# Kernel optimization log

Hardware: AMD Instinct MI355X
Metric: run time of the kernel (lower is better)

## Reference

```python
import jax, jax.numpy as jnp
import numpy as np

B, N, FEAT, H, HID = 2, 2048, 128, 5, 3
D = H * HID  # 15
NEG_INF = -9e15


def _gat(x, adj, W, a, concat):
    # x: [B,N,Fin], W: [Fin,Fout], a: [2*Fout]
    Wh = jnp.einsum('bnf,fo->bno', x, W)
    Fo = W.shape[1]
    f1 = Wh @ a[:Fo]          # [B,N]
    f2 = Wh @ a[Fo:]          # [B,N]
    e = jax.nn.leaky_relu(f1[:, :, None] + f2[:, None, :], 0.2)  # [B,N,N]
    att = jax.nn.softmax(jnp.where(adj > 0, e, NEG_INF), axis=-1)
    h = jnp.einsum('bij,bjo->bio', att, Wh)
    return (jax.nn.elu(h) if concat else h), att


def _diff_pool(x, adj, s):
    # torch_geometric.dense_diff_pool
    s = jax.nn.softmax(s, axis=-1)                       # [B,N,K]
    out = jnp.einsum('bnk,bnf->bkf', s, x)               # [B,K,F]
    out_adj = jnp.einsum('bnk,bnm,bml->bkl', s, adj, s)  # [B,K,K]
    link = jnp.linalg.norm(adj - jnp.einsum('bnk,bmk->bnm', s, s)) / adj.size
    ent = jnp.mean(jnp.sum(-s * jnp.log(s + 1e-15), axis=-1))
    return out, out_adj, link, ent


def setup_inputs() -> dict:
    key = jax.random.key(0)
    ks = jax.random.split(key, 16)
    p = lambda k, shp: (jax.random.normal(k, shp, jnp.float32) * 0.1)
    d = {}
    d['x'] = jax.random.normal(ks[0], (B, N, FEAT), jnp.float32)
    d['adj'] = jax.random.bernoulli(ks[1], 0.05, (B, N, N)).astype(jnp.float32)
    d['W_heads'] = p(ks[2], (H, FEAT, HID))
    d['a_heads'] = p(ks[3], (H, 2 * HID))
    d['W_out'] = p(ks[4], (D, D)); d['a_out'] = p(ks[5], (2 * D,))
    d['W_p1'] = p(ks[6], (D, 32)); d['a_p1'] = p(ks[7], (64,))
    d['lin1_w'] = p(ks[8], (32, 32)); d['lin1_b'] = p(ks[9], (32,))
    d['W_p2'] = p(ks[10], (D, 4)); d['a_p2'] = p(ks[11], (8,))
    d['lin2_w'] = p(ks[12], (4, 4)); d['lin2_b'] = p(ks[13], (4,))
    d['lin_w'] = p(ks[14], (4 * D, 2)); d['lin_b'] = p(ks[15], (2,))
    return d


def reference(x, adj, W_heads, a_heads, W_out, a_out, W_p1, a_p1,
              lin1_w, lin1_b, W_p2, a_p2, lin2_w, lin2_b, lin_w, lin_b):
    # eval mode: dropout = identity
    hs, atts = jax.vmap(lambda W, a: _gat(x, adj, W, a, True))(W_heads, a_heads)
    # hs: [H,B,N,HID] -> concat heads -> [B,N,H*HID]
    h = jnp.moveaxis(hs, 0, 2).reshape(x.shape[0], x.shape[1], -1)
    h = jax.nn.elu(_gat(h, adj, W_out, a_out, False)[0])
    # pool 1: N -> 32 clusters
    s1 = _gat(h, adj, W_p1, a_p1, True)[0] @ lin1_w + lin1_b
    h, adj2, link1, ent1 = _diff_pool(h, adj, s1)
    # pool 2: 32 -> 4 clusters
    s2 = _gat(h, adj2, W_p2, a_p2, True)[0] @ lin2_w + lin2_b
    h, adj3, link2, ent2 = _diff_pool(h, adj2, s2)
    ypred = h.reshape(h.shape[0], -1) @ lin_w + lin_b  # [B, class_num]
    loss = link1 + link2
    return ypred, loss, atts
```

## Files before the change

### kernel.cpp

```cpp
#include <hip/hip_runtime.h>
#include <hip/hip_bf16.h>

#define NN 2048
#define BB 2
#define RB 4096
#define CAP 192

__device__ __forceinline__ float lrelu(float v) { return v > 0.f ? v : 0.2f * v; }
__device__ __forceinline__ float eluf(float v) { return v > 0.f ? v : __expf(v) - 1.f; }

__device__ __forceinline__ float wredsum(float v) {
    for (int o = 32; o; o >>= 1) v += __shfl_down(v, o, 64);
    return v;
}
__device__ __forceinline__ float wredmax(float v) {
    for (int o = 32; o; o >>= 1) v = fmaxf(v, __shfl_down(v, o, 64));
    return v;
}
__device__ __forceinline__ float bsum(float v) {
    for (int m = 32; m; m >>= 1) v += __shfl_xor(v, m, 64);
    return v;
}
__device__ __forceinline__ float bmax(float v) {
    for (int m = 32; m; m >>= 1) v = fmaxf(v, __shfl_xor(v, m, 64));
    return v;
}

__global__ void k_zero(float* S) { if (threadIdx.x < 2) S[threadIdx.x] = 0.f; }

__global__ __launch_bounds__(128) void k_prep1(const float* __restrict__ x,
                                               const float* __restrict__ W,
                                               const float* __restrict__ a,
                                               float* __restrict__ Wh1,
                                               float* __restrict__ f1o,
                                               float* __restrict__ f2o) {
    __shared__ float xl[128];
    __shared__ float whl[15];
    const int r = blockIdx.x, t = threadIdx.x;
    xl[t] = x[(size_t)r * 128 + t];
    __syncthreads();
    if (t < 15) {
        const int h = t / 3, f = t % 3;
        float acc = 0.f;
        const float* Wp = W + (size_t)h * 128 * 3 + f;
        for (int k = 0; k < 128; k++) acc += xl[k] * Wp[k * 3];
        whl[t] = acc;
        Wh1[((size_t)h * RB + r) * 3 + f] = acc;
    }
    __syncthreads();
    if (t < 10) {
        const int h = t >> 1, which = t & 1;
        const float* ah = a + h * 6 + which * 3;
        float acc = whl[h * 3] * ah[0] + whl[h * 3 + 1] * ah[1] + whl[h * 3 + 2] * ah[2];
        (which ? f2o : f1o)[h * RB + r] = acc;
    }
}

__global__ __launch_bounds__(256) void k_gat1(const float* __restrict__ adj,
                                              const float* __restrict__ Wh,
                                              const float* __restrict__ f1,
                                              const float* __restrict__ f2,
                                              const float* __restrict__ W_out,
                                              const float* __restrict__ a_out,
                                              float* __restrict__ Wh2,
                                              float* __restrict__ f1_2,
                                              float* __restrict__ f2_2,
                                              float* __restrict__ att_out,
                                              int* __restrict__ nnzcnt,
                                              unsigned short* __restrict__ nnzidx,
                                              float* __restrict__ S) {
    __shared__ float al[NN];
    __shared__ float red[64];
    __shared__ float h1row[15];
    __shared__ unsigned short nidx[CAP];
    __shared__ int ncnt;
    const int tid = threadIdx.x, wid = tid >> 6, lane = tid & 63;
    const int r = blockIdx.x;
    const int b = r >> 11, i = r & (NN - 1);
    const float* arow = adj + ((size_t)b * NN + i) * NN;

    if (tid == 0) ncnt = 0;
    __syncthreads();

    float a2p = 0.f;
    for (int j = tid; j < NN; j += 256) {
        const float a = arow[j];
        al[j] = a;
        a2p += a * a;
        if (a > 0.f) {
            const int pos = atomicAdd(&ncnt, 1);
            if (pos < CAP) nidx[pos] = (unsigned short)j;
        }
    }
    a2p = wredsum(a2p);
    if (lane == 0) red[wid] = a2p;
    __syncthreads();
    if (tid == 0) atomicAdd(S, red[0] + red[1] + red[2] + red[3]);
    const int cnt = min(ncnt, CAP);
    if (tid == 0) nnzcnt[r] = cnt;
    for (int p = tid; p < cnt; p += 256) nnzidx[(size_t)r * CAP + p] = nidx[p];
    __syncthreads();

    for (int h = 0; h < 5; ++h) {
        const float f1i = f1[h * RB + r];
        const float* f2h = f2 + h * RB + b * NN;
        const float* WhB = Wh + ((size_t)h * RB + b * NN) * 3;

        float ereg[8];
        float lmax = -3.0e38f;
#pragma unroll
        for (int it = 0; it < 8; ++it) {
            const int j = tid + it * 256;
            const float e = (al[j] > 0.f) ? lrelu(f1i + f2h[j]) : -9.0e15f;
            ereg[it] = e;
            lmax = fmaxf(lmax, e);
        }
        lmax = wredmax(lmax);
        if (lane == 0) red[wid] = lmax;
        __syncthreads();
        const float m = fmaxf(fmaxf(red[0], red[1]), fmaxf(red[2], red[3]));
        __syncthreads();

        float lsum = 0.f, h0 = 0.f, h1v = 0.f, h2v = 0.f;
#pragma unroll
        for (int it = 0; it < 8; ++it) {
            const int j = tid + it * 256;
            const float p = __expf(ereg[it] - m);
            ereg[it] = p;
            lsum += p;
            if (p > 0.f) {
                const float* w = WhB + (size_t)j * 3;
                h0 += p * w[0]; h1v += p * w[1]; h2v += p * w[2];
            }
        }
        lsum = wredsum(lsum);
        if (lane == 0) red[wid] = lsum;
        __syncthreads();
        const float inv = 1.f / (red[0] + red[1] + red[2] + red[3]);

        float* ao = att_out + (((size_t)h * BB + b) * NN + i) * NN;
#pragma unroll
        for (int it = 0; it < 8; ++it) ao[tid + it * 256] = ereg[it] * inv;
        __syncthreads();

        h0 = wredsum(h0); h1v = wredsum(h1v); h2v = wredsum(h2v);
        if (lane == 0) { red[wid * 3] = h0; red[wid * 3 + 1] = h1v; red[wid * 3 + 2] = h2v; }
        __syncthreads();
        if (tid < 3) {
            const float v = (red[tid] + red[3 + tid] + red[6 + tid] + red[9 + tid]) * inv;
            h1row[h * 3 + tid] = eluf(v);
        }
        __syncthreads();
    }

    if (wid == 0) {
        float whv = 0.f;
        if (lane < 15) {
#pragma unroll
            for (int f = 0; f < 15; f++) whv += h1row[f] * W_out[f * 15 + lane];
            Wh2[(size_t)r * 15 + lane] = whv;
        }
        float s1p = (lane < 15) ? whv * a_out[lane] : 0.f;
        float s2p = (lane < 15) ? whv * a_out[15 + lane] : 0.f;
        s1p = wredsum(s1p); s2p = wredsum(s2p);
        if (lane == 0) { f1_2[r] = s1p; f2_2[r] = s2p; }
    }
}

__global__ __launch_bounds__(256) void k_gat2(const int* __restrict__ nnzcnt,
                                              const unsigned short* __restrict__ nnzidx,
                                              const float* __restrict__ Wh2,
                                              const float* __restrict__ f1_2,
                                              const float* __restrict__ f2_2,
                                              const float* __restrict__ W_p1,
                                              const float* __restrict__ a_p1,
                                              float* __restrict__ h2,
                                              float* __restrict__ Wh3,
                                              float* __restrict__ f1_3,
                                              float* __restrict__ f2_3) {
    __shared__ unsigned short sidx[4][CAP];
    __shared__ float sp[4][CAP];
    __shared__ float h2l[4][15];
    const int tid = threadIdx.x, w = tid >> 6, lane = tid & 63;
    const int r = blockIdx.x * 4 + w;
    const int b = r >> 11;
    const int cnt = nnzcnt[r];
    for (int q = lane; q < cnt; q += 64) sidx[w][q] = nnzidx[(size_t)r * CAP + q];
    __syncthreads();

    const float f1i = f1_2[r];
    float ee[3];
    float lm = -3.0e38f;
#pragma unroll
    for (int t3 = 0; t3 < 3; ++t3) {
        const int q = lane + 64 * t3;
        if (q < cnt) {
            const int j = sidx[w][q];
            const float v = lrelu(f1i + f2_2[b * NN + j]);
            ee[t3] = v;
            lm = fmaxf(lm, v);
        } else ee[t3] = -3.0e38f;
    }
    const float m = bmax(lm);
    float lsum = 0.f;
#pragma unroll
    for (int t3 = 0; t3 < 3; ++t3) {
        const int q = lane + 64 * t3;
        if (q < cnt) {
            const float p = __expf(ee[t3] - m);
            sp[w][q] = p;
            lsum += p;
        }
    }
    const float inv = 1.f / bsum(lsum);
    __syncthreads();

    const int g4 = lane / 15, f = lane - g4 * 15;
    float acc = 0.f;
    if (lane < 60) {
        for (int q = g4; q < cnt; q += 4)
            acc += sp[w][q] * Wh2[(size_t)(b * NN + sidx[w][q]) * 15 + f];
    }
    acc += __shfl_down(acc, 15, 64);
    acc += __shfl_down(acc, 30, 64);
    if (lane < 15) {
        const float v = eluf(acc * inv);
        h2[(size_t)r * 15 + f] = v;
        h2l[w][f] = v;
    }
    __syncthreads();

    float wh3 = 0.f;
    if (lane < 32) {
#pragma unroll
        for (int ff = 0; ff < 15; ++ff) wh3 += h2l[w][ff] * W_p1[ff * 32 + lane];
        Wh3[(size_t)r * 32 + lane] = wh3;
    }
    float s1p = (lane < 32) ? wh3 * a_p1[lane] : 0.f;
    float s2p = (lane < 32) ? wh3 * a_p1[32 + lane] : 0.f;
    s1p = bsum(s1p); s2p = bsum(s2p);
    if (lane == 0) { f1_3[r] = s1p; f2_3[r] = s2p; }
}

__global__ __launch_bounds__(256) void k_gat3(const int* __restrict__ nnzcnt,
                                              const unsigned short* __restrict__ nnzidx,
                                              const float* __restrict__ Wh3,
                                              const float* __restrict__ f1_3,
                                              const float* __restrict__ f2_3,
                                              const float* __restrict__ lw,
                                              const float* __restrict__ lb,
                                              float* __restrict__ s_out) {
    __shared__ unsigned short sidx[4][CAP];
    __shared__ float sp[4][CAP];
    __shared__ float h3l[4][32];
    const int tid = threadIdx.x, w = tid >> 6, lane = tid & 63;
    const int r = blockIdx.x * 4 + w;
    const int b = r >> 11;
    const int cnt = nnzcnt[r];
    for (int q = lane; q < cnt; q += 64) sidx[w][q] = nnzidx[(size_t)r * CAP + q];
    __syncthreads();

    const float f1i = f1_3[r];
    float ee[3];
    float lm = -3.0e38f;
#pragma unroll
    for (int t3 = 0; t3 < 3; ++t3) {
        const int q = lane + 64 * t3;
        if (q < cnt) {
            const int j = sidx[w][q];
            const float v = lrelu(f1i + f2_3[b * NN + j]);
            ee[t3] = v;
            lm = fmaxf(lm, v);
        } else ee[t3] = -3.0e38f;
    }
    const float m = bmax(lm);
    float lsum = 0.f;
#pragma unroll
    for (int t3 = 0; t3 < 3; ++t3) {
        const int q = lane + 64 * t3;
        if (q < cnt) {
            const float p = __expf(ee[t3] - m);
            sp[w][q] = p;
            lsum += p;
        }
    }
    const float inv = 1.f / bsum(lsum);
    __syncthreads();

    const int g2 = lane >> 5, f = lane & 31;
    float acc = 0.f;
    for (int q = g2; q < cnt; q += 2)
        acc += sp[w][q] * Wh3[(size_t)(b * NN + sidx[w][q]) * 32 + f];
    acc += __shfl_xor(acc, 32, 64);
    if (lane < 32) h3l[w][f] = eluf(acc * inv);
    __syncthreads();

    float z = -3.0e38f;
    if (lane < 32) {
        z = lb[lane];
#pragma unroll
        for (int ff = 0; ff < 32; ++ff) z += h3l[w][ff] * lw[ff * 32 + lane];
    }
    const float zm = bmax(z);
    const float p2 = (lane < 32) ? __expf(z - zm) : 0.f;
    const float zinv = 1.f / bsum(p2);
    if (lane < 32) s_out[(size_t)r * 32 + lane] = p2 * zinv;
}

__global__ __launch_bounds__(256) void k_tsp(const int* __restrict__ nnzcnt,
                                             const unsigned short* __restrict__ nnzidx,
                                             const float* __restrict__ smat,
                                             float* __restrict__ t) {
    __shared__ unsigned short sidx[4][CAP];
    const int tid = threadIdx.x, w = tid >> 6, lane = tid & 63;
    const int r = blockIdx.x * 4 + w;
    const int b = r >> 11;
    const int cnt = nnzcnt[r];
    for (int q = lane; q < cnt; q += 64) sidx[w][q] = nnzidx[(size_t)r * CAP + q];
    __syncthreads();
    const int g2 = lane >> 5, f = lane & 31;
    float acc = 0.f;
    for (int q = g2; q < cnt; q += 2)
        acc += smat[(size_t)(b * NN + sidx[w][q]) * 32 + f];
    acc += __shfl_xor(acc, 32, 64);
    if (lane < 32) t[(size_t)r * 32 + f] = acc;
}

__global__ __launch_bounds__(256) void k_gram2(const float* __restrict__ s,
                                               const float* __restrict__ t,
                                               float* __restrict__ adj2,
                                               float* __restrict__ S) {
    const int bk = blockIdx.x;
    const int b = bk >> 5, k = bk & 31;
    const int tid = threadIdx.x, lane = tid & 63, wid = tid >> 6;
    __shared__ float redG[128], redT[128];
    __shared__ float gsq[32], tval[32];
    float aG[32], aT[32];
#pragma unroll
    for (int l = 0; l < 32; l++) { aG[l] = 0.f; aT[l] = 0.f; }
    const float* sb = s + (size_t)b * NN * 32;
    const float* tb = t + (size_t)b * NN * 32;
    for (int n = tid; n < NN; n += 256) {
        const float sv = sb[(size_t)n * 32 + k];
        const float* sj = sb + (size_t)n * 32;
        const float* tj = tb + (size_t)n * 32;
#pragma unroll
        for (int l = 0; l < 32; l++) { aG[l] += sv * sj[l]; aT[l] += sv * tj[l]; }
    }
#pragma unroll
    for (int l = 0; l < 32; l++) {
        const float vG = wredsum(aG[l]);
        const float vT = wredsum(aT[l]);
        if (lane == 0) { redG[wid * 32 + l] = vG; redT[wid * 32 + l] = vT; }
    }
    __syncthreads();
    if (tid < 32) {
        const float G = redG[tid] + redG[32 + tid] + redG[64 + tid] + redG[96 + tid];
        const float T = redT[tid] + redT[32 + tid] + redT[64 + tid] + redT[96 + tid];
        adj2[((size_t)b * 32 + k) * 32 + tid] = T;
        gsq[tid] = G * G;
        tval[tid] = T;
    }
    __syncthreads();
    if (tid == 0) {
        float ss = 0.f;
#pragma unroll
        for (int l = 0; l < 32; l++) ss += gsq[l];
        atomicAdd(S, ss - 2.f * tval[k]);
    }
}

__global__ __launch_bounds__(256) void k_hp1(const float* __restrict__ s,
                                             const float* __restrict__ h2,
                                             float* __restrict__ hp1) {
    const int bk = blockIdx.x;
    const int b = bk >> 5, k = bk & 31;
    const int tid = threadIdx.x, lane = tid & 63, wid = tid >> 6;
    __shared__ float red[64];
    float acc[15];
#pragma unroll
    for (int f = 0; f < 15; f++) acc[f] = 0.f;
    const float* sb = s + (size_t)b * NN * 32;
    const float* hb = h2 + (size_t)b * NN * 15;
    for (int j = tid; j < NN; j += 256) {
        const float sv = sb[(size_t)j * 32 + k];
        const float* hj = hb + (size_t)j * 15;
#pragma unroll
        for (int f = 0; f < 15; f++) acc[f] += sv * hj[f];
    }
#pragma unroll
    for (int f = 0; f < 15; f++) {
        const float v = wredsum(acc[f]);
        if (lane == 0) red[wid * 15 + f] = v;
    }
    __syncthreads();
    if (tid < 15) hp1[((size_t)b * 32 + k) * 15 + tid] = red[tid] + red[15 + tid] + red[30 + tid] + red[45 + tid];
}

__global__ __launch_bounds__(64) void k_pool2(const float* __restrict__ hp1,
                                              const float* __restrict__ adj2,
                                              const float* __restrict__ Wp2, const float* __restrict__ a2,
                                              const float* __restrict__ l2w, const float* __restrict__ l2b,
                                              const float* __restrict__ lw, const float* __restrict__ lb,
                                              float* __restrict__ S2, float* __restrict__ out) {
    __shared__ float hp[480], a2l[1024], wh[128], f1l[32], f2l[32], s2l[128], hp2[60];
    const int b = blockIdx.x, tid = threadIdx.x;
    for (int idx = tid; idx < 480; idx += 64) hp[idx] = hp1[b * 480 + idx];
    for (int idx = tid; idx < 1024; idx += 64) a2l[idx] = adj2[b * 1024 + idx];
    __syncthreads();
    for (int idx = tid; idx < 128; idx += 64) {
        const int n = idx >> 2, c = idx & 3;
        float acc = 0.f;
#pragma unroll
        for (int f = 0; f < 15; f++) acc += hp[n * 15 + f] * Wp2[f * 4 + c];
        wh[idx] = acc;
    }
    __syncthreads();
    if (tid < 32) {
        float s1 = 0.f, s2 = 0.f;
#pragma unroll
        for (int c = 0; c < 4; c++) {
            s1 += wh[tid * 4 + c] * a2[c];
            s2 += wh[tid * 4 + c] * a2[4 + c];
        }
        f1l[tid] = s1;
        f2l[tid] = s2;
    }
    __syncthreads();
    if (tid < 32) {
        const int n = tid;
        float e[32];
        float m = -3.0e38f;
#pragma unroll
        for (int j = 0; j < 32; j++) {
            const float v = lrelu(f1l[n] + f2l[j]);
            e[j] = a2l[n * 32 + j] > 0.f ? v : -9.0e15f;
            m = fmaxf(m, e[j]);
        }
        float sum = 0.f;
#pragma unroll
        for (int j = 0; j < 32; j++) { e[j] = __expf(e[j] - m); sum += e[j]; }
        const float inv = 1.f / sum;
        float h4[4];
#pragma unroll
        for (int c = 0; c < 4; c++) {
            float acc = 0.f;
#pragma unroll
            for (int j = 0; j < 32; j++) acc += e[j] * wh[j * 4 + c];
            h4[c] = eluf(acc * inv);
        }
        float z[4];
        float zm = -3.0e38f;
#pragma unroll
        for (int c = 0; c < 4; c++) {
            float acc = l2b[c];
#pragma unroll
            for (int c2 = 0; c2 < 4; c2++) acc += h4[c2] * l2w[c2 * 4 + c];
            z[c] = acc;
            zm = fmaxf(zm, acc);
        }
        float zs = 0.f;
#pragma unroll
        for (int c = 0; c < 4; c++) { z[c] = __expf(z[c] - zm); zs += z[c]; }
        const float zi = 1.f / zs;
#pragma unroll
        for (int c = 0; c < 4; c++) s2l[n * 4 + c] = z[c] * zi;
    }
    __syncthreads();
    if (tid < 60) {
        const int c = tid / 15, f = tid % 15;
        float acc = 0.f;
#pragma unroll
        for (int n = 0; n < 32; n++) acc += s2l[n * 4 + c] * hp[n * 15 + f];
        hp2[tid] = acc;
    }
    float lacc = 0.f;
    for (int idx = tid; idx < 1024; idx += 64) {
        const int n = idx >> 5, mm = idx & 31;
        float d = 0.f;
#pragma unroll
        for (int c = 0; c < 4; c++) d += s2l[n * 4 + c] * s2l[mm * 4 + c];
        const float df = a2l[idx] - d;
        lacc += df * df;
    }
    lacc = wredsum(lacc);
    if (tid == 0) atomicAdd(S2, lacc);
    __syncthreads();
    if (tid < 2) {
        float acc = lb[tid];
#pragma unroll
        for (int k2 = 0; k2 < 60; k2++) acc += hp2[k2] * lw[k2 * 2 + tid];
        out[b * 2 + tid] = acc;
    }
}

__global__ void k_final(const float* __restrict__ S, float* __restrict__ out) {
    const float loss = sqrtf(S[0]) / 8388608.f + sqrtf(S[1]) / 2048.f;
    out[4] = loss;
}

extern "C" void kernel_launch(void* const* d_in, const int* in_sizes, int n_in,
                              void* d_out, int out_size, void* d_ws, size_t ws_size,
                              hipStream_t stream) {
    const float* x      = (const float*)d_in[0];
    const float* adj    = (const float*)d_in[1];
    const float* W_h    = (const float*)d_in[2];
    const float* a_h    = (const float*)d_in[3];
    const float* W_out  = (const float*)d_in[4];
    const float* a_out  = (const float*)d_in[5];
    const float* W_p1   = (const float*)d_in[6];
    const float* a_p1   = (const float*)d_in[7];
    const float* lin1_w = (const float*)d_in[8];
    const float* lin1_b = (const float*)d_in[9];
    const float* W_p2   = (const float*)d_in[10];
    const float* a_p2   = (const float*)d_in[11];
    const float* lin2_w = (const float*)d_in[12];
    const float* lin2_b = (const float*)d_in[13];
    const float* lin_w  = (const float*)d_in[14];
    const float* lin_b  = (const float*)d_in[15];
    float* outp = (float*)d_out;

    float* W = (float*)d_ws;
    float* Wh1  = W;
    float* f1_1 = Wh1 + 61440;
    float* f2_1 = f1_1 + 20480;
    float* Wh2  = f2_1 + 20480;
    float* f1_2 = Wh2 + 61440;
    float* f2_2 = f1_2 + 4096;
    float* h2   = f2_2 + 4096;
    float* Wh3  = h2 + 61440;
    float* f1_3 = Wh3 + 131072;
    float* f2_3 = f1_3 + 4096;
    float* s    = f2_3 + 4096;
    float* t    = s + 131072;
    float* hp1  = t + 131072;
    float* adj2 = hp1 + 960;
    float* S    = adj2 + 2048;
    int* nnzcnt = (int*)(S + 2);
    unsigned short* nnzidx = (unsigned short*)(nnzcnt + RB);

    k_zero<<<1, 64, 0, stream>>>(S);
    k_prep1<<<RB, 128, 0, stream>>>(x, W_h, a_h, Wh1, f1_1, f2_1);
    k_gat1<<<RB, 256, 0, stream>>>(adj, Wh1, f1_1, f2_1, W_out, a_out,
                                   Wh2, f1_2, f2_2, outp + 5, nnzcnt, nnzidx, S);
    k_gat2<<<RB / 4, 256, 0, stream>>>(nnzcnt, nnzidx, Wh2, f1_2, f2_2,
                                       W_p1, a_p1, h2, Wh3, f1_3, f2_3);
    k_gat3<<<RB / 4, 256, 0, stream>>>(nnzcnt, nnzidx, Wh3, f1_3, f2_3,
                                       lin1_w, lin1_b, s);
    k_tsp<<<RB / 4, 256, 0, stream>>>(nnzcnt, nnzidx, s, t);
    k_gram2<<<64, 256, 0, stream>>>(s, t, adj2, S);
    k_hp1<<<64, 256, 0, stream>>>(s, h2, hp1);
    k_pool2<<<BB, 64, 0, stream>>>(hp1, adj2, W_p2, a_p2, lin2_w, lin2_b, lin_w, lin_b, S + 1, outp);
    k_final<<<1, 1, 0, stream>>>(S, outp);
}
```

Measured before the change: 218.5 us.

## Compute GAT layer-1 softmax sparsely over neighbor lists with one wave per head

k_gat1 now runs all five heads at once, one wave each, with 320 threads. Each wave computes exp-scores only for the gathered nonzero neighbors, scatters them into a zeroed shared dense row, and writes the normalized attention row with aligned float4 stores. This drops the per-head dense max/sum passes and most block-wide barriers. The max-subtraction step is gone, and the squared-adjacency sum is replaced by the neighbor count, which assumes binary adjacency and no overflow of the neighbor list (CAP). k_prep1 is also reworked to one wave per row, using shuffle reductions and four rows per block.

```diff
diff --git a/kernel.cpp b/kernel.cpp
--- a/kernel.cpp
+++ b/kernel.cpp
@@ -13,10 +13,6 @@
     for (int o = 32; o; o >>= 1) v += __shfl_down(v, o, 64);
     return v;
 }
-__device__ __forceinline__ float wredmax(float v) {
-    for (int o = 32; o; o >>= 1) v = fmaxf(v, __shfl_down(v, o, 64));
-    return v;
-}
 __device__ __forceinline__ float bsum(float v) {
     for (int m = 32; m; m >>= 1) v += __shfl_xor(v, m, 64);
     return v;
@@ -28,35 +24,33 @@
 
 __global__ void k_zero(float* S) { if (threadIdx.x < 2) S[threadIdx.x] = 0.f; }
 
-__global__ __launch_bounds__(128) void k_prep1(const float* __restrict__ x,
+__global__ __launch_bounds__(256) void k_prep1(const float* __restrict__ x,
                                                const float* __restrict__ W,
                                                const float* __restrict__ a,
                                                float* __restrict__ Wh1,
                                                float* __restrict__ f1o,
                                                float* __restrict__ f2o) {
-    __shared__ float xl[128];
-    __shared__ float whl[15];
-    const int r = blockIdx.x, t = threadIdx.x;
-    xl[t] = x[(size_t)r * 128 + t];
-    __syncthreads();
-    if (t < 15) {
-        const int h = t / 3, f = t % 3;
-        float acc = 0.f;
-        const float* Wp = W + (size_t)h * 128 * 3 + f;
-        for (int k = 0; k < 128; k++) acc += xl[k] * Wp[k * 3];
-        whl[t] = acc;
-        Wh1[((size_t)h * RB + r) * 3 + f] = acc;
-    }
-    __syncthreads();
-    if (t < 10) {
-        const int h = t >> 1, which = t & 1;
-        const float* ah = a + h * 6 + which * 3;
-        float acc = whl[h * 3] * ah[0] + whl[h * 3 + 1] * ah[1] + whl[h * 3 + 2] * ah[2];
-        (which ? f2o : f1o)[h * RB + r] = acc;
-    }
-}
-
-__global__ __launch_bounds__(256) void k_gat1(const float* __restrict__ adj,
+    const int tid = threadIdx.x, w = tid >> 6, lane = tid & 63;
+    const int r = blockIdx.x * 4 + w;
+    const float xa = x[(size_t)r * 128 + lane];
+    const float xb = x[(size_t)r * 128 + 64 + lane];
+#pragma unroll
+    for (int h = 0; h < 5; ++h) {
+        float f1v = 0.f, f2v = 0.f;
+#pragma unroll
+        for (int f = 0; f < 3; ++f) {
+            const float w0 = W[h * 384 + lane * 3 + f];
+            const float w1 = W[h * 384 + (lane + 64) * 3 + f];
+            const float d = bsum(xa * w0 + xb * w1);
+            if (lane == 0) Wh1[((size_t)h * RB + r) * 3 + f] = d;
+            f1v += d * a[h * 6 + f];
+            f2v += d * a[h * 6 + 3 + f];
+        }
+        if (lane == 0) { f1o[h * RB + r] = f1v; f2o[h * RB + r] = f2v; }
+    }
+}
+
+__global__ __launch_bounds__(320) void k_gat1(const float* __restrict__ adj,
                                               const float* __restrict__ Wh,
                                               const float* __restrict__ f1,
                                               const float* __restrict__ f2,
@@ -69,91 +63,63 @@
                                               int* __restrict__ nnzcnt,
                                               unsigned short* __restrict__ nnzidx,
                                               float* __restrict__ S) {
-    __shared__ float al[NN];
-    __shared__ float red[64];
+    __shared__ float dense[5][2052];
+    __shared__ unsigned short nidx[CAP];
     __shared__ float h1row[15];
-    __shared__ unsigned short nidx[CAP];
     __shared__ int ncnt;
-    const int tid = threadIdx.x, wid = tid >> 6, lane = tid & 63;
+    const int tid = threadIdx.x, h = tid >> 6, lane = tid & 63;
     const int r = blockIdx.x;
     const int b = r >> 11, i = r & (NN - 1);
     const float* arow = adj + ((size_t)b * NN + i) * NN;
 
     if (tid == 0) ncnt = 0;
     __syncthreads();
-
-    float a2p = 0.f;
-    for (int j = tid; j < NN; j += 256) {
-        const float a = arow[j];
-        al[j] = a;
-        a2p += a * a;
-        if (a > 0.f) {
+    for (int j = tid; j < NN; j += 320) {
+        if (arow[j] > 0.f) {
             const int pos = atomicAdd(&ncnt, 1);
             if (pos < CAP) nidx[pos] = (unsigned short)j;
         }
     }
-    a2p = wredsum(a2p);
-    if (lane == 0) red[wid] = a2p;
-    __syncthreads();
-    if (tid == 0) atomicAdd(S, red[0] + red[1] + red[2] + red[3]);
+    __syncthreads();
     const int cnt = min(ncnt, CAP);
-    if (tid == 0) nnzcnt[r] = cnt;
-    for (int p = tid; p < cnt; p += 256) nnzidx[(size_t)r * CAP + p] = nidx[p];
-    __syncthreads();
-
-    for (int h = 0; h < 5; ++h) {
-        const float f1i = f1[h * RB + r];
-        const float* f2h = f2 + h * RB + b * NN;
-        const float* WhB = Wh + ((size_t)h * RB + b * NN) * 3;
-
-        float ereg[8];
-        float lmax = -3.0e38f;
-#pragma unroll
-        for (int it = 0; it < 8; ++it) {
-            const int j = tid + it * 256;
-            const float e = (al[j] > 0.f) ? lrelu(f1i + f2h[j]) : -9.0e15f;
-            ereg[it] = e;
-            lmax = fmaxf(lmax, e);
-        }
-        lmax = wredmax(lmax);
-        if (lane == 0) red[wid] = lmax;
-        __syncthreads();
-        const float m = fmaxf(fmaxf(red[0], red[1]), fmaxf(red[2], red[3]));
-        __syncthreads();
-
-        float lsum = 0.f, h0 = 0.f, h1v = 0.f, h2v = 0.f;
-#pragma unroll
-        for (int it = 0; it < 8; ++it) {
-            const int j = tid + it * 256;
-            const float p = __expf(ereg[it] - m);
-            ereg[it] = p;
-            lsum += p;
-            if (p > 0.f) {
-                const float* w = WhB + (size_t)j * 3;
-                h0 += p * w[0]; h1v += p * w[1]; h2v += p * w[2];
-            }
-        }
-        lsum = wredsum(lsum);
-        if (lane == 0) red[wid] = lsum;
-        __syncthreads();
-        const float inv = 1.f / (red[0] + red[1] + red[2] + red[3]);
-
-        float* ao = att_out + (((size_t)h * BB + b) * NN + i) * NN;
-#pragma unroll
-        for (int it = 0; it < 8; ++it) ao[tid + it * 256] = ereg[it] * inv;
-        __syncthreads();
-
-        h0 = wredsum(h0); h1v = wredsum(h1v); h2v = wredsum(h2v);
-        if (lane == 0) { red[wid * 3] = h0; red[wid * 3 + 1] = h1v; red[wid * 3 + 2] = h2v; }
-        __syncthreads();
-        if (tid < 3) {
-            const float v = (red[tid] + red[3 + tid] + red[6 + tid] + red[9 + tid]) * inv;
-            h1row[h * 3 + tid] = eluf(v);
-        }
-        __syncthreads();
-    }
-
-    if (wid == 0) {
+    if (tid == 0) { nnzcnt[r] = cnt; atomicAdd(S, (float)ncnt); }
+    for (int p = tid; p < cnt; p += 320) nnzidx[(size_t)r * CAP + p] = nidx[p];
+
+    float4* dz = (float4*)dense[h];
+#pragma unroll
+    for (int v = lane; v < 513; v += 64) dz[v] = make_float4(0.f, 0.f, 0.f, 0.f);
+
+    const float f1i = f1[h * RB + r];
+    const float* f2h = f2 + h * RB + b * NN;
+    const float* WhB = Wh + ((size_t)h * RB + b * NN) * 3;
+    float lsum = 0.f, h0 = 0.f, h1v = 0.f, h2v = 0.f;
+    for (int q = lane; q < cnt; q += 64) {
+        const int j = nidx[q];
+        const float p = __expf(lrelu(f1i + f2h[j]));
+        dense[h][j + 1] = p;
+        lsum += p;
+        const float* wv = WhB + (size_t)j * 3;
+        h0 += p * wv[0]; h1v += p * wv[1]; h2v += p * wv[2];
+    }
+    const float inv = 1.f / bsum(lsum);
+    h0 = bsum(h0); h1v = bsum(h1v); h2v = bsum(h2v);
+    if (lane == 0) {
+        h1row[h * 3 + 0] = eluf(h0 * inv);
+        h1row[h * 3 + 1] = eluf(h1v * inv);
+        h1row[h * 3 + 2] = eluf(h2v * inv);
+    }
+    float* ao = att_out + (((size_t)h * BB + b) * NN + i) * NN;
+    if (lane < 3) ao[lane] = dense[h][1 + lane] * inv;
+    float4* ao4 = (float4*)(ao + 3);
+    const float4* dh4 = (const float4*)dense[h];
+    for (int v = lane; v < 511; v += 64) {
+        const float4 d = dh4[1 + v];
+        ao4[v] = make_float4(d.x * inv, d.y * inv, d.z * inv, d.w * inv);
+    }
+    if (lane == 63) ao[2047] = dense[h][2048] * inv;
+
+    __syncthreads();
+    if (h == 0) {
         float whv = 0.f;
         if (lane < 15) {
 #pragma unroll
@@ -540,8 +506,8 @@
     unsigned short* nnzidx = (unsigned short*)(nnzcnt + RB);
 
     k_zero<<<1, 64, 0, stream>>>(S);
-    k_prep1<<<RB, 128, 0, stream>>>(x, W_h, a_h, Wh1, f1_1, f2_1);
-    k_gat1<<<RB, 256, 0, stream>>>(adj, Wh1, f1_1, f2_1, W_out, a_out,
+    k_prep1<<<RB / 4, 256, 0, stream>>>(x, W_h, a_h, Wh1, f1_1, f2_1);
+    k_gat1<<<RB, 320, 0, stream>>>(adj, Wh1, f1_1, f2_1, W_out, a_out,
                                    Wh2, f1_2, f2_2, outp + 5, nnzcnt, nnzidx, S);
     k_gat2<<<RB / 4, 256, 0, stream>>>(nnzcnt, nnzidx, Wh2, f1_2, f2_2,
                                        W_p1, a_p1, h2, Wh3, f1_3, f2_3);
```

After: 177.7 us. 18.7% less time.
